# Optimization experiments

Hardware: AMD Instinct MI355X
Metric: run time of the kernel (lower is better)

Reference implementation:

```python
import jax, jax.numpy as jnp
import numpy as np

B, C, H, W = 16, 2048, 16, 16
HEADS = 4
HEAD_DIM = C // HEADS


def setup_inputs() -> dict:
    key = jax.random.key(0)
    ks = jax.random.split(key, 7)
    s = 0.02
    x = jax.random.normal(ks[0], (B, C, H, W), dtype=jnp.float32)
    q_w = jax.random.normal(ks[1], (HEADS, HEAD_DIM, C), dtype=jnp.float32) * s
    q_b = jax.random.normal(ks[2], (HEADS, HEAD_DIM), dtype=jnp.float32) * s
    k_w = jax.random.normal(ks[3], (HEADS, HEAD_DIM, C), dtype=jnp.float32) * s
    k_b = jax.random.normal(ks[4], (HEADS, HEAD_DIM), dtype=jnp.float32) * s
    v_w = jax.random.normal(ks[5], (HEADS, C, C), dtype=jnp.float32) * s
    v_b = jax.random.normal(ks[6], (HEADS, C), dtype=jnp.float32) * s
    return {"x": x, "q_w": q_w, "q_b": q_b, "k_w": k_w, "k_b": k_b, "v_w": v_w, "v_b": v_b}


def reference(x, q_w, q_b, k_w, k_b, v_w, v_b):
    b, c, h, w = x.shape
    heads, head_dim, _ = q_w.shape
    # [B, N, C] with N = H*W
    patch = jnp.transpose(x, (0, 2, 3, 1)).reshape(b, h * w, c)
    # stacked per-head linear projections (bias per head)
    Q = jnp.einsum('bnc,hdc->bhnd', patch, q_w) + q_b[None, :, None, :]   # [B,heads,N,head_dim]
    K = jnp.einsum('bnc,hdc->bhnd', patch, k_w) + k_b[None, :, None, :]   # [B,heads,N,head_dim]
    V = jnp.einsum('bnc,hec->bhne', patch, v_w) + v_b[None, :, None, :]   # [B,heads,N,C]
    sim = jnp.einsum('bhqd,bhkd->bhqk', Q, K) / (head_dim ** 0.5)          # [B,heads,N,N]
    # sum over query dim, softmax over heads
    att = jnp.sum(sim, axis=2)[:, :, None, :]                              # [B,heads,1,N]
    att = jax.nn.softmax(att, axis=1)
    n = att.shape[-1]
    side = int(n ** 0.5)
    attention_score = att.reshape(b, heads, side, side)                    # [B,heads,h,w]
    # per-head spatial gating of the input, concatenated along channels
    x_enhance = (attention_score[:, :, None, :, :] * x[:, None, :, :, :]).reshape(b, heads * c, h, w)
    # standard softmax attention combine
    sim = jax.nn.softmax(sim, axis=-1)
    general = jnp.einsum('bhqk,bhke->bhqe', sim, V)                        # [B,heads,N,C]
    general = general.reshape(b, heads, side, side, c)
    general = jnp.transpose(general, (0, 1, 4, 2, 3)).reshape(b, heads * c, side, side)
    output = general + x_enhance
    return (attention_score, output)
```

## Files before the change

### kernel.cpp

```cpp
#include <hip/hip_runtime.h>
#include <hip/hip_bf16.h>
#include <hip/hip_fp8.h>

#define B_ 16
#define C_ 2048
#define N_ 256
#define HEADS_ 4
#define D_ 512

typedef unsigned int u32;
typedef unsigned char u8;
typedef unsigned short ushort_t;
typedef __attribute__((ext_vector_type(8))) short bfx8;
typedef __attribute__((ext_vector_type(4))) float fx4;

__device__ __forceinline__ unsigned short f2bs(float f) {
    __hip_bfloat16 h = __float2bfloat16(f);
    return __builtin_bit_cast(unsigned short, h);
}
__device__ __forceinline__ float bs2f(ushort_t u) {
    u32 v = ((u32)u) << 16;
    return __builtin_bit_cast(float, v);
}
__device__ __forceinline__ u8 f2f8(float f) {
    return (u8)__hip_cvt_float_to_fp8(f, __HIP_SATFINITE, __HIP_E4M3);
}
__device__ __forceinline__ void gload16(const void* g, void* l) {
    __builtin_amdgcn_global_load_lds((const __attribute__((address_space(1))) u32*)g,
                                     (__attribute__((address_space(3))) u32*)l, 16, 0, 0);
}
__device__ __forceinline__ int xcd_swz(int bid, int nwg) {
    return (bid & 7) * (nwg >> 3) + (bid >> 3);
}

#define SBAR() __builtin_amdgcn_s_barrier()
#define LGKM0() do { asm volatile("s_waitcnt lgkmcnt(0)" ::: "memory"); \
                     __builtin_amdgcn_sched_barrier(0); } while (0)

#define VMW4() asm volatile("s_waitcnt vmcnt(4)" ::: "memory")

#define STAGEF8(MAT, BUF, KH, J) do {                                         \
    const u8* s_ = (MAT) ? Bm : A;                                            \
    const int r_ = tid >> 1;                                                  \
    const int k_ = (J) * 64 + (KH) * 32 + (((tid & 1) ^ ((tid >> 3) & 1)) * 16); \
    gload16(s_ + (size_t)r_ * K + k_,                                         \
            (u8*)(&lds[MAT][BUF][KH][0][0]) + tid * 16);                      \
} while (0)

#define LDAF8(dst, BUF, KH, MH) do {                                          \
    _Pragma("unroll")                                                         \
    for (int i_ = 0; i_ < 4; ++i_)                                            \
        dst[i_] = *(const long*)(&lds[0][BUF][KH][wmr + (MH) * 64 + i_ * 16 + l16][f8off]); \
} while (0)

#define LDBF8(dst, BUF, KH) do {                                              \
    _Pragma("unroll")                                                         \
    for (int i_ = 0; i_ < 4; ++i_)                                            \
        dst[i_] = *(const long*)(&lds[1][BUF][KH][wnr + i_ * 16 + l16][f8off]); \
} while (0)

#define MMF8(aa, bb, MH) do {                                                 \
    _Pragma("unroll")                                                         \
    for (int i_ = 0; i_ < 4; ++i_) {                                          \
        _Pragma("unroll")                                                     \
        for (int n_ = 0; n_ < 4; ++n_)                                        \
            acc[(MH) * 4 + i_][n_] = __builtin_amdgcn_mfma_f32_16x16x32_fp8_fp8( \
                aa[i_], bb[n_], acc[(MH) * 4 + i_][n_], 0, 0, 0);             \
    }                                                                         \
} while (0)

#define KTILE2F8(BUF, JS1, JS2) do {                                          \
    long a0[4], a1[4], b0[4];                                                 \
                                 \
    LDAF8(a0, BUF, 0, 0); LDAF8(a1, BUF, 0, 1); LDBF8(b0, BUF, 0);            \
    STAGEF8(0, BUF ^ 1, 1, JS1);                                              \
    STAGEF8(1, BUF ^ 1, 1, JS1);                                              \
    SBAR(); LGKM0();                                                          \
    __builtin_amdgcn_s_setprio(1);                                            \
    MMF8(a0, b0, 0); MMF8(a1, b0, 1);                                         \
    __builtin_amdgcn_s_setprio(0);                                            \
    VMW4();                                                                   \
    SBAR();                                                                   \
                                           \
    LDAF8(a0, BUF, 1, 0); LDAF8(a1, BUF, 1, 1); LDBF8(b0, BUF, 1);            \
    STAGEF8(0, BUF, 0, JS2);                                                  \
    STAGEF8(1, BUF, 0, JS2);                                                  \
    SBAR(); LGKM0();                                                          \
    __builtin_amdgcn_s_setprio(1);                                            \
    MMF8(a0, b0, 0); MMF8(a1, b0, 1);                                         \
    __builtin_amdgcn_s_setprio(0);                                            \
    VMW4();                                                                   \
    SBAR();                                                                   \
} while (0)

typedef u8 ldsf8_t[2][2][2][256][32];

__device__ __forceinline__ void gemm256_f8(const u8* __restrict__ A,
                                           const u8* __restrict__ Bm,
                                           int K, ldsf8_t& lds, fx4 acc[8][4])
{
    const int tid = threadIdx.x;
    const int lane = tid & 63;
    const int w = tid >> 6;
    const int l16 = lane & 15, lhi = lane >> 4;
    const int f8off = (((lhi >> 1) ^ ((l16 >> 2) & 1)) * 16) + (lhi & 1) * 8;
    const int wmr = (w >> 2) * 128;
    const int wnr = (w & 3) * 64;
    const int nkt = K >> 6;

    STAGEF8(0, 0, 0, 0); STAGEF8(1, 0, 0, 0);
    STAGEF8(0, 0, 1, 0); STAGEF8(1, 0, 1, 0);
    STAGEF8(0, 1, 0, 1); STAGEF8(1, 1, 0, 1);
    VMW4();
    SBAR();

    for (int jj = 0; jj < nkt; jj += 2) {
        const int js1a = jj + 1;
        const int js2a = (jj + 2 < nkt) ? jj + 2 : nkt - 1;
        const int js1b = js2a;
        const int js2b = (jj + 3 < nkt) ? jj + 3 : nkt - 1;
        KTILE2F8(0, js1a, js2a);
        KTILE2F8(1, js1b, js2b);
    }
    asm volatile("s_waitcnt vmcnt(0)" ::: "memory");
    SBAR();
}

#define EPI256_IDX() \
    const int lane = threadIdx.x & 63, w = threadIdx.x >> 6; \
    const int l16 = lane & 15, lhi = lane >> 4; \
    const int wmr = (w >> 2) * 128, wnr = (w & 3) * 64;

__device__ __forceinline__ void mfma_core(const ushort_t* __restrict__ A,
                                          const ushort_t* __restrict__ Bm,
                                          int K, fx4 acc[4][4])
{
    __shared__ __align__(16) ushort_t As[128 * 32];
    __shared__ __align__(16) ushort_t Bs[128 * 32];
    const int tid = threadIdx.x;
    const int lane = tid & 63, wave = tid >> 6;
    const int l16 = lane & 15, lhi = lane >> 4;
    const int swz8 = (lhi ^ ((l16 >> 1) & 3)) * 8;
    const int wm = (wave >> 1) * 64, wn = (wave & 1) * 64;

    for (int k0 = 0; k0 < K; k0 += 32) {
        const int f0 = tid, f1 = tid + 256;
        gload16(A + (size_t)(f0 >> 2) * K + k0 + (((f0 & 3) ^ ((f0 >> 3) & 3)) * 8), As + f0 * 8);
        gload16(A + (size_t)(f1 >> 2) * K + k0 + (((f1 & 3) ^ ((f1 >> 3) & 3)) * 8), As + f1 * 8);
        gload16(Bm + (size_t)(f0 >> 2) * K + k0 + (((f0 & 3) ^ ((f0 >> 3) & 3)) * 8), Bs + f0 * 8);
        gload16(Bm + (size_t)(f1 >> 2) * K + k0 + (((f1 & 3) ^ ((f1 >> 3) & 3)) * 8), Bs + f1 * 8);
        __syncthreads();
        bfx8 af[4], bfr[4];
#pragma unroll
        for (int i = 0; i < 4; ++i)
            af[i] = *(const bfx8*)(As + (wm + i * 16 + l16) * 32 + swz8);
#pragma unroll
        for (int j = 0; j < 4; ++j)
            bfr[j] = *(const bfx8*)(Bs + (wn + j * 16 + l16) * 32 + swz8);
#pragma unroll
        for (int i = 0; i < 4; ++i)
#pragma unroll
            for (int j = 0; j < 4; ++j)
                acc[i][j] = __builtin_amdgcn_mfma_f32_16x16x32_bf16(af[i], bfr[j], acc[i][j], 0, 0, 0);
        __syncthreads();
    }
}

#define EPI_IDX() \
    const int lane = threadIdx.x & 63, wave = threadIdx.x >> 6; \
    const int l16 = lane & 15, lhi = lane >> 4; \
    const int wm = (wave >> 1) * 64, wn = (wave & 1) * 64;

__global__ __launch_bounds__(256) void k_castw8(const float* __restrict__ s, u8* __restrict__ d,
                                                int n, float scale) {
    int i = (blockIdx.x * 256 + threadIdx.x) * 4;
    if (i >= n) return;
    float4 v = *(const float4*)(s + i);
    uchar4 o = { f2f8(v.x * scale), f2f8(v.y * scale), f2f8(v.z * scale), f2f8(v.w * scale) };
    *(uchar4*)(d + i) = o;
}

__global__ __launch_bounds__(256) void k_cast_x(const float* __restrict__ x,
                                                ushort_t* __restrict__ xb, u8* __restrict__ xb8,
                                                u8* __restrict__ xbT8, float* __restrict__ xpart) {
    __shared__ float t[32][33];
    const int b = blockIdx.z, c0 = blockIdx.y * 32, n0 = blockIdx.x * 32;
    const int tn = threadIdx.x & 31, tc8 = threadIdx.x >> 5;
    const float* xp = x + ((size_t)b * C_ + c0) * N_ + n0;
#pragma unroll
    for (int p = 0; p < 4; ++p) {
        int cc = tc8 + p * 8;
        float v = xp[(size_t)cc * N_ + tn];
        t[cc][tn] = v;
        xb[((size_t)b * C_ + c0 + cc) * N_ + n0 + tn] = f2bs(v);
        xb8[((size_t)b * C_ + c0 + cc) * N_ + n0 + tn] = f2f8(v * 8.0f);
        float s = v;
#pragma unroll
        for (int o = 16; o; o >>= 1) s += __shfl_xor(s, o, 32);
        if (tn == 0) xpart[(size_t)blockIdx.x * B_ * C_ + (size_t)b * C_ + c0 + cc] = s;
    }
    __syncthreads();
#pragma unroll
    for (int p = 0; p < 4; ++p) {
        int nn = tc8 + p * 8;
        xbT8[((size_t)b * N_ + n0 + nn) * C_ + c0 + tn] = f2f8(t[tn][nn] * 8.0f);
    }
}

__global__ __launch_bounds__(256) void k_xsum2(const float* __restrict__ xpart, float* __restrict__ xsum) {
    const int c = blockIdx.x * 256 + threadIdx.x, b = blockIdx.y;
    float s = 0.f;
#pragma unroll
    for (int t = 0; t < 8; ++t) s += xpart[(size_t)t * B_ * C_ + (size_t)b * C_ + c];
    xsum[(size_t)b * C_ + c] = s;
}

__global__ __launch_bounds__(256) void k_qsum(const float* __restrict__ xsum, const float* __restrict__ qw,
                                              const float* __restrict__ qb, float* __restrict__ qsum) {
    const int wave = threadIdx.x >> 6, lane = threadIdx.x & 63;
    const int row = blockIdx.x * 4 + wave;
    const int h = row >> 9, d = row & 511;
    const float* wr = qw + (size_t)row * C_;
    float acc[16];
#pragma unroll
    for (int bb = 0; bb < 16; ++bb) acc[bb] = 0.f;
    for (int it = 0; it < C_ / 64; ++it) {
        const int c = it * 64 + lane;
        const float w = wr[c];
#pragma unroll
        for (int bb = 0; bb < 16; ++bb) acc[bb] += xsum[(size_t)bb * C_ + c] * w;
    }
#pragma unroll
    for (int bb = 0; bb < 16; ++bb) {
        float s = acc[bb];
#pragma unroll
        for (int o = 32; o; o >>= 1) s += __shfl_xor(s, o, 64);
        if (lane == 0) qsum[(size_t)((bb << 2) | h) * D_ + d] = s + 256.0f * qb[row];
    }
}

__global__ __launch_bounds__(64) void k_const(const float* __restrict__ qsum, const float* __restrict__ kb,
                                              float* __restrict__ cst) {
    const int bh = blockIdx.x, h = bh & 3, lane = threadIdx.x;
    float s = 0.f;
    for (int d = lane; d < D_; d += 64) s += qsum[(size_t)bh * D_ + d] * kb[h * D_ + d];
#pragma unroll
    for (int o = 32; o; o >>= 1) s += __shfl_xor(s, o, 64);
    if (lane == 0) cst[bh] = s;
}

__global__ __launch_bounds__(256) void k_vecp(const float* __restrict__ qsum, const float* __restrict__ kw,
                                              float* __restrict__ partv) {
    const int ct = blockIdx.x, h = blockIdx.y, dsl = blockIdx.z;
    __shared__ float qs[16 * 128];
    for (int i = threadIdx.x; i < 16 * 128; i += 256) {
        int bb = i >> 7, dd = i & 127;
        qs[i] = qsum[(size_t)((bb << 2) | h) * D_ + dsl * 128 + dd];
    }
    __syncthreads();
    const int c = ct * 256 + threadIdx.x;
    const float* wp = kw + ((size_t)h * D_ + dsl * 128) * C_ + c;
    float acc[16];
#pragma unroll
    for (int bb = 0; bb < 16; ++bb) acc[bb] = 0.f;
    for (int dd = 0; dd < 128; ++dd) {
        const float w = wp[(size_t)dd * C_];
#pragma unroll
        for (int bb = 0; bb < 16; ++bb) acc[bb] += qs[bb * 128 + dd] * w;
    }
#pragma unroll
    for (int bb = 0; bb < 16; ++bb)
        partv[((size_t)dsl * 64 + ((bb << 2) | h)) * C_ + c] = acc[bb];
}

__global__ __launch_bounds__(256) void k_att(const float* __restrict__ x, const float* __restrict__ partv,
                                             float* __restrict__ part) {
    const int bh = blockIdx.x, sl = blockIdx.y, b = bh >> 2;
    __shared__ float vs[512];
    const int c0 = sl * 512;
    for (int i = threadIdx.x; i < 512; i += 256) {
        float v = 0.f;
#pragma unroll
        for (int dsl = 0; dsl < 4; ++dsl) v += partv[((size_t)dsl * 64 + bh) * C_ + c0 + i];
        vs[i] = v;
    }
    __syncthreads();
    float a = 0.f;
    const float* xp = x + ((size_t)b * C_ + c0) * N_ + threadIdx.x;
#pragma unroll 8
    for (int c = 0; c < 512; ++c) a += vs[c] * xp[(size_t)c * N_];
    part[((size_t)sl * 64 + bh) * N_ + threadIdx.x] = a;
}

__global__ __launch_bounds__(256) void k_score(const float* __restrict__ part, const float* __restrict__ cst,
                                               float* __restrict__ score, float* __restrict__ out0) {
    const int b = blockIdx.x, k = threadIdx.x;
    const float scale = 0.044194173824159216f;
    float a[4];
#pragma unroll
    for (int h = 0; h < 4; ++h) {
        const int bh = b * 4 + h;
        float s = cst[bh];
#pragma unroll
        for (int sl = 0; sl < 4; ++sl) s += part[((size_t)sl * 64 + bh) * N_ + k];
        a[h] = s * scale;
    }
    float mx = fmaxf(fmaxf(a[0], a[1]), fmaxf(a[2], a[3]));
    float e0 = expf(a[0] - mx), e1 = expf(a[1] - mx), e2 = expf(a[2] - mx), e3 = expf(a[3] - mx);
    float inv = 1.0f / (e0 + e1 + e2 + e3);
    float r[4] = { e0 * inv, e1 * inv, e2 * inv, e3 * inv };
#pragma unroll
    for (int h = 0; h < 4; ++h) {
        score[(size_t)(b * 4 + h) * N_ + k] = r[h];
        out0[(size_t)(b * 4 + h) * N_ + k] = r[h];
    }
}

__global__ __launch_bounds__(512, 2) void k_proj(const u8* __restrict__ xbT8,
                                                 const u8* __restrict__ qw8, const u8* __restrict__ kw8,
                                                 const float* __restrict__ qb, const float* __restrict__ kb,
                                                 ushort_t* __restrict__ QKbuf) {
    __shared__ __align__(16) ldsf8_t lds;
    const int wg = xcd_swz(blockIdx.x, 256);
    const int quad = wg >> 2;
    const int mt = quad >> 2;
    const int nt = (quad & 3) * 4 + (wg & 3);
    const int c0 = nt * 256;
    const int qk = c0 >> 11;
    const int rem = c0 & 2047;
    const u8* A  = xbT8 + (size_t)mt * 256 * C_;
    const u8* Bm = (qk ? kw8 : qw8) + (size_t)rem * C_;
    const float* bias  = (qk ? kb : qb) + rem;
    const int K = C_;

    fx4 acc[8][4];
#pragma unroll
    for (int i = 0; i < 8; ++i)
#pragma unroll
        for (int j = 0; j < 4; ++j) acc[i][j] = (fx4){0.f, 0.f, 0.f, 0.f};
    gemm256_f8(A, Bm, K, lds, acc);

    EPI256_IDX();
#pragma unroll
    for (int i = 0; i < 8; ++i)
#pragma unroll
        for (int n = 0; n < 4; ++n)
#pragma unroll
            for (int r = 0; r < 4; ++r) {
                const int gr = mt * 256 + wmr + i * 16 + lhi * 4 + r;
                const int bq = gr >> 8, nn = gr & 255;
                const int lc = wnr + n * 16 + l16;
                const int hh = (rem + lc) >> 9, dl = (rem + lc) & 511;
                const float v = acc[i][n][r] * (1.0f / 512.0f) + bias[lc];
                QKbuf[((((size_t)(qk * 16 + bq) * 4 + hh) * 256) + nn) * 512 + dl] = f2bs(v);
            }
}

__global__ __launch_bounds__(512, 2) void k_out(const u8* __restrict__ vw8, const float* __restrict__ vb,
                                                const u8* __restrict__ Tt8, const float* __restrict__ score,
                                                const ushort_t* __restrict__ xb, float* __restrict__ out1) {
    __shared__ __align__(16) ldsf8_t lds;
    const int wg = xcd_swz(blockIdx.x, 512);
    const int h = wg >> 7, l = wg & 127;
    const int quad = l >> 2;
    const int mt = quad >> 2;
    const int nt = (quad & 3) * 4 + (l & 3);
    const u8* A  = vw8 + (size_t)h * C_ * C_ + (size_t)mt * 256 * C_;
    const u8* Bm = Tt8 + (size_t)h * 16 * N_ * C_ + (size_t)nt * 256 * C_;
    const int K = C_;

    fx4 acc[8][4];
#pragma unroll
    for (int i = 0; i < 8; ++i)
#pragma unroll
        for (int j = 0; j < 4; ++j) acc[i][j] = (fx4){0.f, 0.f, 0.f, 0.f};
    gemm256_f8(A, Bm, K, lds, acc);

    EPI256_IDX();
#pragma unroll
    for (int i = 0; i < 8; ++i)
#pragma unroll
        for (int n = 0; n < 4; ++n)
#pragma unroll
            for (int r = 0; r < 4; ++r) {
                const int e = mt * 256 + wmr + i * 16 + lhi * 4 + r;
                const int col = nt * 256 + wnr + n * 16 + l16;
                const int b = col >> 8, nn = col & 255;
                float v = acc[i][n][r] * (1.0f / 1024.0f) + vb[h * C_ + e]
                        + score[(size_t)(b * 4 + h) * N_ + nn] * bs2f(xb[((size_t)b * C_ + e) * N_ + nn]);
                out1[((size_t)(b * 4 + h) * C_ + e) * N_ + nn] = v;
            }
}

__global__ __launch_bounds__(512, 2) void k_T8(const u8* __restrict__ Pb8, const u8* __restrict__ xb8,
                                               u8* __restrict__ Tt8) {
    __shared__ __align__(16) ldsf8_t lds;
    const int wg = xcd_swz(blockIdx.x, 512);
    const int b = wg >> 5, l = wg & 31;
    const int mt = l >> 3, nt = l & 7;
    const u8* A  = Pb8 + ((size_t)b * 1024 + mt * 256) * 256;
    const u8* Bm = xb8 + ((size_t)b * 2048 + nt * 256) * 256;
    const int K = N_;

    fx4 acc[8][4];
#pragma unroll
    for (int i = 0; i < 8; ++i)
#pragma unroll
        for (int j = 0; j < 4; ++j) acc[i][j] = (fx4){0.f, 0.f, 0.f, 0.f};
    gemm256_f8(A, Bm, K, lds, acc);

    EPI256_IDX();
#pragma unroll
    for (int i = 0; i < 8; ++i)
#pragma unroll
        for (int n = 0; n < 4; ++n)
#pragma unroll
            for (int r = 0; r < 4; ++r) {
                const int rowm = mt * 256 + wmr + i * 16 + lhi * 4 + r;
                const int h = rowm >> 8, q = rowm & 255;
                const int c = nt * 256 + wnr + n * 16 + l16;
                Tt8[(((size_t)h * 16 + b) * 256 + q) * 2048 + c] = f2f8(acc[i][n][r] * 0.0078125f);
            }
}

__global__ __launch_bounds__(256) void k_sim(const ushort_t* __restrict__ QKbuf, float* __restrict__ simf) {
    const int wg = blockIdx.x;
    const int bh = wg >> 2, mt = (wg >> 1) & 1, ntl = wg & 1;
    const ushort_t* Qr = QKbuf;
    const ushort_t* Kr = QKbuf + (size_t)16 * 4 * 256 * 512;
    const ushort_t* A = Qr + ((size_t)bh * 256 + mt * 128) * 512;
    const ushort_t* Bm = Kr + ((size_t)bh * 256 + ntl * 128) * 512;

    fx4 acc[4][4];
#pragma unroll
    for (int i = 0; i < 4; ++i)
#pragma unroll
        for (int j = 0; j < 4; ++j) acc[i][j] = (fx4){0.f, 0.f, 0.f, 0.f};
    mfma_core(A, Bm, D_, acc);

    EPI_IDX();
    const float scale = 0.044194173824159216f;
#pragma unroll
    for (int i = 0; i < 4; ++i)
#pragma unroll
        for (int j = 0; j < 4; ++j)
#pragma unroll
            for (int r = 0; r < 4; ++r) {
                const int q = mt * 128 + wm + i * 16 + lhi * 4 + r;
                const int k = ntl * 128 + wn + j * 16 + l16;
                simf[(size_t)bh * N_ * N_ + (size_t)q * N_ + k] = acc[i][j][r] * scale;
            }
}

__global__ __launch_bounds__(64) void k_softP(const float* __restrict__ simf, u8* __restrict__ Pb8) {
    const size_t row = blockIdx.x;
    const float* p = simf + row * N_;
    u8* o = Pb8 + row * N_;
    const int t = threadIdx.x;
    float v0 = p[t], v1 = p[t + 64], v2 = p[t + 128], v3 = p[t + 192];
    float mx = fmaxf(fmaxf(v0, v1), fmaxf(v2, v3));
#pragma unroll
    for (int off = 32; off; off >>= 1) mx = fmaxf(mx, __shfl_xor(mx, off, 64));
    float e0 = expf(v0 - mx), e1 = expf(v1 - mx), e2 = expf(v2 - mx), e3 = expf(v3 - mx);
    float s = e0 + e1 + e2 + e3;
#pragma unroll
    for (int off = 32; off; off >>= 1) s += __shfl_xor(s, off, 64);
    const float inv = 256.0f / s;
    o[t] = f2f8(e0 * inv); o[t + 64] = f2f8(e1 * inv);
    o[t + 128] = f2f8(e2 * inv); o[t + 192] = f2f8(e3 * inv);
}

extern "C" void kernel_launch(void* const* d_in, const int* in_sizes, int n_in,
                              void* d_out, int out_size, void* d_ws, size_t ws_size,
                              hipStream_t stream)
{
    const float* x  = (const float*)d_in[0];
    const float* qw = (const float*)d_in[1];
    const float* qb = (const float*)d_in[2];
    const float* kw = (const float*)d_in[3];
    const float* kb = (const float*)d_in[4];
    const float* vw = (const float*)d_in[5];
    const float* vb = (const float*)d_in[6];

    float* out0 = (float*)d_out;
    float* out1 = out0 + (size_t)B_ * HEADS_ * N_;

    char* w = (char*)d_ws;
    u8*       vw8  = (u8*)w;        w += (size_t)4 * C_ * C_;
    u8*       qw8  = (u8*)w;        w += (size_t)4 * D_ * C_;
    u8*       kw8  = (u8*)w;        w += (size_t)4 * D_ * C_;
    ushort_t* xb   = (ushort_t*)w;  w += (size_t)B_ * C_ * N_ * 2;
    u8*       xb8  = (u8*)w;        w += (size_t)B_ * C_ * N_;
    u8*       xbT8 = (u8*)w;        w += (size_t)B_ * N_ * C_;
    ushort_t* QKbuf= (ushort_t*)w;  w += (size_t)2 * 16 * 4 * 256 * 512 * 2;
    u8*       Pb8  = (u8*)w;        w += (size_t)64 * N_ * N_;
    float*    simf = (float*)w;     w += (size_t)64 * N_ * N_ * 4;
    u8*       Tt8  = (u8*)w;        w += (size_t)64 * N_ * C_;
    float*    xpart= (float*)w;     w += (size_t)8 * B_ * C_ * 4;
    float*    xsum = (float*)w;     w += (size_t)B_ * C_ * 4;
    float*    qsum = (float*)w;     w += (size_t)64 * D_ * 4;
    float*    cst  = (float*)w;     w += 1024;
    float*    partv= (float*)w;     w += (size_t)4 * 64 * C_ * 4;
    float*    part = (float*)w;     w += (size_t)4 * 64 * N_ * 4;
    float*    score= (float*)w;     w += (size_t)64 * N_ * 4;

    k_castw8<<<dim3(4 * D_ * C_ / 4 / 256), 256, 0, stream>>>(qw, qw8, 4 * D_ * C_, 64.0f);
    k_castw8<<<dim3(4 * D_ * C_ / 4 / 256), 256, 0, stream>>>(kw, kw8, 4 * D_ * C_, 64.0f);
    k_castw8<<<dim3(4 * C_ * C_ / 4 / 256), 256, 0, stream>>>(vw, vw8, 4 * C_ * C_, 64.0f);
    k_cast_x<<<dim3(8, 64, 16), 256, 0, stream>>>(x, xb, xb8, xbT8, xpart);

    k_xsum2<<<dim3(8, 16), 256, 0, stream>>>(xpart, xsum);
    k_qsum <<<dim3(512), 256, 0, stream>>>(xsum, qw, qb, qsum);
    k_const<<<dim3(64), 64, 0, stream>>>(qsum, kb, cst);
    k_vecp <<<dim3(8, 4, 4), 256, 0, stream>>>(qsum, kw, partv);
    k_att  <<<dim3(64, 4), 256, 0, stream>>>(x, partv, part);
    k_score<<<dim3(16), 256, 0, stream>>>(part, cst, score, out0);

    k_proj <<<dim3(256), 512, 0, stream>>>(xbT8, qw8, kw8, qb, kb, QKbuf);
    k_sim  <<<dim3(256), 256, 0, stream>>>(QKbuf, simf);
    k_softP<<<dim3(64 * N_), 64, 0, stream>>>(simf, Pb8);
    k_T8   <<<dim3(512), 512, 0, stream>>>(Pb8, xb8, Tt8);
    k_out  <<<dim3(512), 512, 0, stream>>>(vw8, vb, Tt8, score, xb, out1);
}
```

Before: 364.3 us.

## Load A operand directly from global into registers, stage only B in LDS

The shared FP8 GEMM core now keeps only the B tile in LDS and has each wave read its A fragments straight from global memory into registers. A is double-buffered across k-tiles (aA/aB) and B uses the LDS double buffer, with the vmcnt wait raised to cover the extra outstanding loads. This halves LDS footprint and LDS read traffic for A and cuts LDS staging for it. In exchange it adds register pressure and uncoalesced 8-byte global loads, and A rows are re-read by the four waves sharing an M half.

```diff
diff --git a/kernel.cpp b/kernel.cpp
--- a/kernel.cpp
+++ b/kernel.cpp
@@ -37,67 +37,64 @@
 #define LGKM0() do { asm volatile("s_waitcnt lgkmcnt(0)" ::: "memory"); \
                      __builtin_amdgcn_sched_barrier(0); } while (0)
 
-#define VMW4() asm volatile("s_waitcnt vmcnt(4)" ::: "memory")
-
-#define STAGEF8(MAT, BUF, KH, J) do {                                         \
-    const u8* s_ = (MAT) ? Bm : A;                                            \
+#define VMW17() asm volatile("s_waitcnt vmcnt(17)" ::: "memory")
+
+#define STAGEB(BUF, KH, J) do {                                               \
     const int r_ = tid >> 1;                                                  \
     const int k_ = (J) * 64 + (KH) * 32 + (((tid & 1) ^ ((tid >> 3) & 1)) * 16); \
-    gload16(s_ + (size_t)r_ * K + k_,                                         \
-            (u8*)(&lds[MAT][BUF][KH][0][0]) + tid * 16);                      \
+    gload16(Bm + (size_t)r_ * K + k_,                                         \
+            (u8*)(&lds[BUF][KH][0][0]) + tid * 16);                           \
 } while (0)
 
-#define LDAF8(dst, BUF, KH, MH) do {                                          \
+#define LDB(dst, BUF, KH) do {                                                \
     _Pragma("unroll")                                                         \
     for (int i_ = 0; i_ < 4; ++i_)                                            \
-        dst[i_] = *(const long*)(&lds[0][BUF][KH][wmr + (MH) * 64 + i_ * 16 + l16][f8off]); \
+        dst[i_] = *(const long*)(&lds[BUF][KH][wnr + i_ * 16 + l16][f8off]);  \
 } while (0)
 
-#define LDBF8(dst, BUF, KH) do {                                              \
+#define ALOAD(dst, J) do {                                                    \
     _Pragma("unroll")                                                         \
-    for (int i_ = 0; i_ < 4; ++i_)                                            \
-        dst[i_] = *(const long*)(&lds[1][BUF][KH][wnr + i_ * 16 + l16][f8off]); \
-} while (0)
-
-#define MMF8(aa, bb, MH) do {                                                 \
+    for (int mf_ = 0; mf_ < 8; ++mf_) {                                       \
+        dst[mf_][0] = *(const long*)(arow + (size_t)mf_ * 16 * K + (J) * 64);      \
+        dst[mf_][1] = *(const long*)(arow + (size_t)mf_ * 16 * K + (J) * 64 + 32); \
+    } } while (0)
+
+#define MM32(av, bb, KH) do {                                                 \
+    __builtin_amdgcn_s_setprio(1);                                            \
     _Pragma("unroll")                                                         \
-    for (int i_ = 0; i_ < 4; ++i_) {                                          \
+    for (int mf_ = 0; mf_ < 8; ++mf_) {                                       \
         _Pragma("unroll")                                                     \
         for (int n_ = 0; n_ < 4; ++n_)                                        \
-            acc[(MH) * 4 + i_][n_] = __builtin_amdgcn_mfma_f32_16x16x32_fp8_fp8( \
-                aa[i_], bb[n_], acc[(MH) * 4 + i_][n_], 0, 0, 0);             \
+            acc[mf_][n_] = __builtin_amdgcn_mfma_f32_16x16x32_fp8_fp8(        \
+                av[mf_][KH], bb[n_], acc[mf_][n_], 0, 0, 0);                  \
     }                                                                         \
+    __builtin_amdgcn_s_setprio(0);                                            \
 } while (0)
 
-#define KTILE2F8(BUF, JS1, JS2) do {                                          \
-    long a0[4], a1[4], b0[4];                                                 \
-                                 \
-    LDAF8(a0, BUF, 0, 0); LDAF8(a1, BUF, 0, 1); LDBF8(b0, BUF, 0);            \
-    STAGEF8(0, BUF ^ 1, 1, JS1);                                              \
-    STAGEF8(1, BUF ^ 1, 1, JS1);                                              \
+#define KTILE_RA(ACUR, ANXT, BUF, JNXT) do {                                  \
+    long b0[4];                                                               \
+                                                           \
+    LDB(b0, BUF, 0);                                                          \
+    STAGEB(BUF ^ 1, 0, JNXT);                                                 \
+    ALOAD(ANXT, JNXT);                                                        \
     SBAR(); LGKM0();                                                          \
-    __builtin_amdgcn_s_setprio(1);                                            \
-    MMF8(a0, b0, 0); MMF8(a1, b0, 1);                                         \
-    __builtin_amdgcn_s_setprio(0);                                            \
-    VMW4();                                                                   \
+    MM32(ACUR, b0, 0);                                                        \
+    VMW17();                                                                  \
     SBAR();                                                                   \
-                                           \
-    LDAF8(a0, BUF, 1, 0); LDAF8(a1, BUF, 1, 1); LDBF8(b0, BUF, 1);            \
-    STAGEF8(0, BUF, 0, JS2);                                                  \
-    STAGEF8(1, BUF, 0, JS2);                                                  \
+                                                           \
+    LDB(b0, BUF, 1);                                                          \
+    STAGEB(BUF ^ 1, 1, JNXT);                                                 \
     SBAR(); LGKM0();                                                          \
-    __builtin_amdgcn_s_setprio(1);                                            \
-    MMF8(a0, b0, 0); MMF8(a1, b0, 1);                                         \
-    __builtin_amdgcn_s_setprio(0);                                            \
-    VMW4();                                                                   \
+    MM32(ACUR, b0, 1);                                                        \
+    VMW17();                                                                  \
     SBAR();                                                                   \
 } while (0)
 
-typedef u8 ldsf8_t[2][2][2][256][32];
-
-__device__ __forceinline__ void gemm256_f8(const u8* __restrict__ A,
-                                           const u8* __restrict__ Bm,
-                                           int K, ldsf8_t& lds, fx4 acc[8][4])
+typedef u8 ldsB_t[2][2][256][32];
+
+__device__ __forceinline__ void gemm256_f8ra(const u8* __restrict__ A,
+                                             const u8* __restrict__ Bm,
+                                             int K, ldsB_t& lds, fx4 acc[8][4])
 {
     const int tid = threadIdx.x;
     const int lane = tid & 63;
@@ -107,20 +104,21 @@
     const int wmr = (w >> 2) * 128;
     const int wnr = (w & 3) * 64;
     const int nkt = K >> 6;
-
-    STAGEF8(0, 0, 0, 0); STAGEF8(1, 0, 0, 0);
-    STAGEF8(0, 0, 1, 0); STAGEF8(1, 0, 1, 0);
-    STAGEF8(0, 1, 0, 1); STAGEF8(1, 1, 0, 1);
-    VMW4();
+    const u8* arow = A + (size_t)(wmr + l16) * K + lhi * 8;
+
+    long aA[8][2], aB[8][2];
+
+    STAGEB(0, 0, 0);
+    STAGEB(0, 1, 0);
+    ALOAD(aA, 0);
+    VMW17();
     SBAR();
 
     for (int jj = 0; jj < nkt; jj += 2) {
-        const int js1a = jj + 1;
-        const int js2a = (jj + 2 < nkt) ? jj + 2 : nkt - 1;
-        const int js1b = js2a;
-        const int js2b = (jj + 3 < nkt) ? jj + 3 : nkt - 1;
-        KTILE2F8(0, js1a, js2a);
-        KTILE2F8(1, js1b, js2b);
+        const int jn1 = jj + 1;
+        const int jn2 = (jj + 2 < nkt) ? jj + 2 : nkt - 1;
+        KTILE_RA(aA, aB, 0, jn1);
+        KTILE_RA(aB, aA, 1, jn2);
     }
     asm volatile("s_waitcnt vmcnt(0)" ::: "memory");
     SBAR();
@@ -320,7 +318,7 @@
                                                  const u8* __restrict__ qw8, const u8* __restrict__ kw8,
                                                  const float* __restrict__ qb, const float* __restrict__ kb,
                                                  ushort_t* __restrict__ QKbuf) {
-    __shared__ __align__(16) ldsf8_t lds;
+    __shared__ __align__(16) ldsB_t lds;
     const int wg = xcd_swz(blockIdx.x, 256);
     const int quad = wg >> 2;
     const int mt = quad >> 2;
@@ -338,7 +336,7 @@
     for (int i = 0; i < 8; ++i)
 #pragma unroll
         for (int j = 0; j < 4; ++j) acc[i][j] = (fx4){0.f, 0.f, 0.f, 0.f};
-    gemm256_f8(A, Bm, K, lds, acc);
+    gemm256_f8ra(A, Bm, K, lds, acc);
 
     EPI256_IDX();
 #pragma unroll
@@ -359,7 +357,7 @@
 __global__ __launch_bounds__(512, 2) void k_out(const u8* __restrict__ vw8, const float* __restrict__ vb,
                                                 const u8* __restrict__ Tt8, const float* __restrict__ score,
                                                 const ushort_t* __restrict__ xb, float* __restrict__ out1) {
-    __shared__ __align__(16) ldsf8_t lds;
+    __shared__ __align__(16) ldsB_t lds;
     const int wg = xcd_swz(blockIdx.x, 512);
     const int h = wg >> 7, l = wg & 127;
     const int quad = l >> 2;
@@ -374,7 +372,7 @@
     for (int i = 0; i < 8; ++i)
 #pragma unroll
         for (int j = 0; j < 4; ++j) acc[i][j] = (fx4){0.f, 0.f, 0.f, 0.f};
-    gemm256_f8(A, Bm, K, lds, acc);
+    gemm256_f8ra(A, Bm, K, lds, acc);
 
     EPI256_IDX();
 #pragma unroll
@@ -394,7 +392,7 @@
 
 __global__ __launch_bounds__(512, 2) void k_T8(const u8* __restrict__ Pb8, const u8* __restrict__ xb8,
                                                u8* __restrict__ Tt8) {
-    __shared__ __align__(16) ldsf8_t lds;
+    __shared__ __align__(16) ldsB_t lds;
     const int wg = xcd_swz(blockIdx.x, 512);
     const int b = wg >> 5, l = wg & 31;
     const int mt = l >> 3, nt = l & 7;
@@ -407,7 +405,7 @@
     for (int i = 0; i < 8; ++i)
 #pragma unroll
         for (int j = 0; j < 4; ++j) acc[i][j] = (fx4){0.f, 0.f, 0.f, 0.f};
-    gemm256_f8(A, Bm, K, lds, acc);
+    gemm256_f8ra(A, Bm, K, lds, acc);
 
     EPI256_IDX();
 #pragma unroll
```

Measured after the change: 669.5 us. +83.8%, slower.

## Use 128x128 fp8 GEMM tiles with 256-thread blocks in output kernel

Applied to the files above, without the earlier changes.

Adds a 128x128 tile fp8 MFMA GEMM routine (4 waves, 64x64 per wave) and switches the k_out V-projection/combine kernel to it, launching 2048 blocks of 256 threads instead of 512 blocks of 512 threads with 256x256 tiles. The aim is more blocks in flight and better occupancy and load balance across CUs. The cost is lower data reuse per tile, so each block moves more global/LDS traffic per unit of MFMA work.

```diff
diff --git a/kernel.cpp b/kernel.cpp
--- a/kernel.cpp
+++ b/kernel.cpp
@@ -36,7 +36,6 @@
 #define SBAR() __builtin_amdgcn_s_barrier()
 #define LGKM0() do { asm volatile("s_waitcnt lgkmcnt(0)" ::: "memory"); \
                      __builtin_amdgcn_sched_barrier(0); } while (0)
-
 #define VMW4() asm volatile("s_waitcnt vmcnt(4)" ::: "memory")
 
 #define STAGEF8(MAT, BUF, KH, J) do {                                         \
@@ -71,7 +70,6 @@
 
 #define KTILE2F8(BUF, JS1, JS2) do {                                          \
     long a0[4], a1[4], b0[4];                                                 \
-                                 \
     LDAF8(a0, BUF, 0, 0); LDAF8(a1, BUF, 0, 1); LDBF8(b0, BUF, 0);            \
     STAGEF8(0, BUF ^ 1, 1, JS1);                                              \
     STAGEF8(1, BUF ^ 1, 1, JS1);                                              \
@@ -81,7 +79,6 @@
     __builtin_amdgcn_s_setprio(0);                                            \
     VMW4();                                                                   \
     SBAR();                                                                   \
-                                           \
     LDAF8(a0, BUF, 1, 0); LDAF8(a1, BUF, 1, 1); LDBF8(b0, BUF, 1);            \
     STAGEF8(0, BUF, 0, JS2);                                                  \
     STAGEF8(1, BUF, 0, JS2);                                                  \
@@ -130,6 +127,81 @@
     const int lane = threadIdx.x & 63, w = threadIdx.x >> 6; \
     const int l16 = lane & 15, lhi = lane >> 4; \
     const int wmr = (w >> 2) * 128, wnr = (w & 3) * 64;
+
+typedef u8 lds128_t[2][2][2][128][32];
+
+#define STG1(MAT, BUF, KH, J) do {                                            \
+    const u8* s_ = (MAT) ? Bm : A;                                            \
+    const int r_ = tid >> 1;                                                  \
+    const int k_ = (J) * 64 + (KH) * 32 + (((tid & 1) ^ ((tid >> 3) & 1)) * 16); \
+    gload16(s_ + (size_t)r_ * K + k_,                                         \
+            (u8*)(&lds[MAT][BUF][KH][0][0]) + tid * 16);                      \
+} while (0)
+
+#define LD1(dst, MAT, BUF, KH, base) do {                                     \
+    _Pragma("unroll")                                                         \
+    for (int i_ = 0; i_ < 4; ++i_)                                            \
+        dst[i_] = *(const long*)(&lds[MAT][BUF][KH][(base) + i_ * 16 + l16][f8off]); \
+} while (0)
+
+#define MM16(aa, bb) do {                                                     \
+    __builtin_amdgcn_s_setprio(1);                                            \
+    _Pragma("unroll")                                                         \
+    for (int i_ = 0; i_ < 4; ++i_) {                                          \
+        _Pragma("unroll")                                                     \
+        for (int n_ = 0; n_ < 4; ++n_)                                        \
+            acc[i_][n_] = __builtin_amdgcn_mfma_f32_16x16x32_fp8_fp8(         \
+                aa[i_], bb[n_], acc[i_][n_], 0, 0, 0);                        \
+    }                                                                         \
+    __builtin_amdgcn_s_setprio(0);                                            \
+} while (0)
+
+#define KT128(BUF, JS1, JS2) do {                                             \
+    long a0[4], b0[4];                                                        \
+    LD1(a0, 0, BUF, 0, wm); LD1(b0, 1, BUF, 0, wn);                           \
+    STG1(0, BUF ^ 1, 1, JS1); STG1(1, BUF ^ 1, 1, JS1);                       \
+    SBAR(); LGKM0();                                                          \
+    MM16(a0, b0);                                                             \
+    VMW4();                                                                   \
+    SBAR();                                                                   \
+    LD1(a0, 0, BUF, 1, wm); LD1(b0, 1, BUF, 1, wn);                           \
+    STG1(0, BUF, 0, JS2); STG1(1, BUF, 0, JS2);                               \
+    SBAR(); LGKM0();                                                          \
+    MM16(a0, b0);                                                             \
+    VMW4();                                                                   \
+    SBAR();                                                                   \
+} while (0)
+
+__device__ __forceinline__ void gemm128_f8(const u8* __restrict__ A,
+                                           const u8* __restrict__ Bm,
+                                           int K, lds128_t& lds, fx4 acc[4][4])
+{
+    const int tid = threadIdx.x;
+    const int lane = tid & 63;
+    const int w = tid >> 6;
+    const int l16 = lane & 15, lhi = lane >> 4;
+    const int f8off = (((lhi >> 1) ^ ((l16 >> 2) & 1)) * 16) + (lhi & 1) * 8;
+    const int wm = (w >> 1) * 64;
+    const int wn = (w & 1) * 64;
+    const int nkt = K >> 6;
+
+    STG1(0, 0, 0, 0); STG1(1, 0, 0, 0);
+    STG1(0, 0, 1, 0); STG1(1, 0, 1, 0);
+    STG1(0, 1, 0, 1); STG1(1, 1, 0, 1);
+    VMW4();
+    SBAR();
+
+    for (int jj = 0; jj < nkt; jj += 2) {
+        const int js1a = jj + 1;
+        const int js2a = (jj + 2 < nkt) ? jj + 2 : nkt - 1;
+        const int js1b = js2a;
+        const int js2b = (jj + 3 < nkt) ? jj + 3 : nkt - 1;
+        KT128(0, js1a, js2a);
+        KT128(1, js1b, js2b);
+    }
+    asm volatile("s_waitcnt vmcnt(0)" ::: "memory");
+    SBAR();
+}
 
 __device__ __forceinline__ void mfma_core(const ushort_t* __restrict__ A,
                                           const ushort_t* __restrict__ Bm,
@@ -356,35 +428,35 @@
             }
 }
 
-__global__ __launch_bounds__(512, 2) void k_out(const u8* __restrict__ vw8, const float* __restrict__ vb,
+__global__ __launch_bounds__(256, 3) void k_out(const u8* __restrict__ vw8, const float* __restrict__ vb,
                                                 const u8* __restrict__ Tt8, const float* __restrict__ score,
                                                 const ushort_t* __restrict__ xb, float* __restrict__ out1) {
-    __shared__ __align__(16) ldsf8_t lds;
-    const int wg = xcd_swz(blockIdx.x, 512);
-    const int h = wg >> 7, l = wg & 127;
-    const int quad = l >> 2;
-    const int mt = quad >> 2;
-    const int nt = (quad & 3) * 4 + (l & 3);
-    const u8* A  = vw8 + (size_t)h * C_ * C_ + (size_t)mt * 256 * C_;
-    const u8* Bm = Tt8 + (size_t)h * 16 * N_ * C_ + (size_t)nt * 256 * C_;
+    __shared__ __align__(16) lds128_t lds;
+    const int wg = xcd_swz(blockIdx.x, 2048);
+    const int h = wg >> 9, l = wg & 511;
+    const int mt = l >> 5, nt = l & 31;
+    const u8* A  = vw8 + (size_t)h * C_ * C_ + (size_t)mt * 128 * C_;
+    const u8* Bm = Tt8 + (size_t)h * 16 * N_ * C_ + (size_t)nt * 128 * C_;
     const int K = C_;
 
-    fx4 acc[8][4];
-#pragma unroll
-    for (int i = 0; i < 8; ++i)
+    fx4 acc[4][4];
+#pragma unroll
+    for (int i = 0; i < 4; ++i)
 #pragma unroll
         for (int j = 0; j < 4; ++j) acc[i][j] = (fx4){0.f, 0.f, 0.f, 0.f};
-    gemm256_f8(A, Bm, K, lds, acc);
-
-    EPI256_IDX();
-#pragma unroll
-    for (int i = 0; i < 8; ++i)
+    gemm128_f8(A, Bm, K, lds, acc);
+
+    const int lane = threadIdx.x & 63, w = threadIdx.x >> 6;
+    const int l16 = lane & 15, lhi = lane >> 4;
+    const int wm = (w >> 1) * 64, wn = (w & 1) * 64;
+#pragma unroll
+    for (int i = 0; i < 4; ++i)
 #pragma unroll
         for (int n = 0; n < 4; ++n)
 #pragma unroll
             for (int r = 0; r < 4; ++r) {
-                const int e = mt * 256 + wmr + i * 16 + lhi * 4 + r;
-                const int col = nt * 256 + wnr + n * 16 + l16;
+                const int e = mt * 128 + wm + i * 16 + lhi * 4 + r;
+                const int col = nt * 128 + wn + n * 16 + l16;
                 const int b = col >> 8, nn = col & 255;
                 float v = acc[i][n][r] * (1.0f / 1024.0f) + vb[h * C_ + e]
                         + score[(size_t)(b * 4 + h) * N_ + nn] * bs2f(xb[((size_t)b * C_ + e) * N_ + nn]);
@@ -520,5 +592,5 @@
     k_sim  <<<dim3(256), 256, 0, stream>>>(QKbuf, simf);
     k_softP<<<dim3(64 * N_), 64, 0, stream>>>(simf, Pb8);
     k_T8   <<<dim3(512), 512, 0, stream>>>(Pb8, xb8, Tt8);
-    k_out  <<<dim3(512), 512, 0, stream>>>(vw8, vb, Tt8, score, xb, out1);
-}
+    k_out  <<<dim3(2048), 256, 0, stream>>>(vw8, vb, Tt8, score, xb, out1);
+}
```

After: 388.3 us. 6.6% more time.
